# Kernel tuning notes

Hardware: AMD Instinct MI355X
Metric: run time of the kernel (lower is better)

## Reference

```python
import jax, jax.numpy as jnp
import numpy as np

N, E, T = 25000, 400000, 4          # nodes, edges, edge types (one-hot width)
NODE_DIM, EDGE_DIM = 128, 64        # raw feature dims
NO, EO, OUT = 32, 64, 128           # node_ft_out_dim, edge_ft_out_dim, out_dim
D = NO + EO + NO                    # z_node_lv_dim = 128


def segment_softmax(scores, seg, num_segments):
    """Numerically stable softmax over variable-sized segments (1D scores)."""
    m = jax.ops.segment_max(scores, seg, num_segments=num_segments)
    ex = jnp.exp(scores - m[seg])
    den = jax.ops.segment_sum(ex, seg, num_segments=num_segments)
    return ex / den[seg]


def setup_inputs() -> dict:
    key = jax.random.key(0)
    ks = jax.random.split(key, 11)
    node_features = jax.random.normal(ks[0], (N, NODE_DIM), dtype=jnp.float32)
    edge_features = jax.random.normal(ks[1], (E, EDGE_DIM), dtype=jnp.float32)
    src = jax.random.randint(ks[2], (E,), 0, N, dtype=jnp.int32)
    dst = jax.random.randint(ks[3], (E,), 0, N, dtype=jnp.int32)
    edge_type_idx = jax.random.randint(ks[4], (E,), 0, T, dtype=jnp.int32)
    # learned params (torch Linear stored transposed: we use [in, out])
    W_n = jax.random.normal(ks[5], (NODE_DIM, NO), dtype=jnp.float32) / np.sqrt(NODE_DIM)
    W_e = jax.random.normal(ks[6], (EDGE_DIM, EO), dtype=jnp.float32) / np.sqrt(EDGE_DIM)
    w_eattn = jax.random.normal(ks[7], (EO + NO,), dtype=jnp.float32) / np.sqrt(EO + NO)
    w_attn = jax.random.normal(ks[8], (D,), dtype=jnp.float32) / np.sqrt(D)
    w_sem = jax.random.normal(ks[9], (D,), dtype=jnp.float32) / np.sqrt(D)
    W_fc2 = jax.random.normal(ks[10], (D, OUT), dtype=jnp.float32) / np.sqrt(D)
    return {
        "node_features": node_features, "edge_features": edge_features,
        "src": src, "dst": dst, "edge_type_idx": edge_type_idx,
        "W_n": W_n, "W_e": W_e, "w_eattn": w_eattn, "w_attn": w_attn,
        "w_sem": w_sem, "W_fc2": W_fc2,
    }


def reference(node_features, edge_features, src, dst, edge_type_idx,
              W_n, W_e, w_eattn, w_attn, w_sem, W_fc2):
    n = node_features.shape[0]
    # --- WeightedAggEdge: project, then softmax edge weights grouped by SRC ---
    z = node_features @ W_n                      # [N, NO]
    e_ft = edge_features @ W_e                   # [E, EO]
    z_src = z[src]                               # [E, NO]
    s1 = jax.nn.leaky_relu(jnp.concatenate([e_ft, z_src], axis=1) @ w_eattn)  # [E]
    gamma = segment_softmax(s1, src, n)          # softmax over edges sharing src
    e_w = gamma[:, None] * e_ft                  # [E, EO]
    # --- BaseGAT_Modified: edge attention + softmax over DST mailboxes ---
    z_dst = z[dst]                               # [E, NO]
    # message z == z2 == [src z, e_weighted, dst z]
    msg = jnp.concatenate([z_src, e_w, z_dst], axis=1)   # [E, D]
    s2 = jax.nn.leaky_relu(msg @ w_attn)         # [E]
    alpha = segment_softmax(s2, dst, n)          # softmax over incoming edges
    weighted = alpha[:, None] * msg              # [E, D]
    # type-grouped scatter-sum: out[dst, t] += onehot(type)[t] * weighted
    seg = dst * T + edge_type_idx                # fused (node, type) segment id
    h = jax.ops.segment_sum(weighted, seg, num_segments=n * T).reshape(n, T, D)
    # --- SemLevelGAT: semantic attention over edge types ---
    zphi = h.sum(axis=0)                         # [T, D]
    beta = jax.nn.softmax(jax.nn.leaky_relu(zphi @ w_sem))   # [T]
    Z = jnp.einsum('t,ntd->nd', beta, h) @ W_fc2             # [N, OUT]
    return Z, e_w
```

## Files before the change

kernel.cpp:

```cpp
#include <hip/hip_runtime.h>

#define NN 25000
#define NE 400000
#define TT 4
#define NO 32
#define EO 64
#define DD 128
#define OUTD 128
#define EGRID 1250
#define REDB (EGRID / 25)

#define OFF_Z      0
#define OFF_ASRC   800000
#define OFF_BSRC   825000
#define OFF_BDST   850000
#define OFF_ZPART  875000
#define OFF_C2     1400000
#define OFF_S1X    1800000
#define OFF_GAMMA  2200000
#define OFF_S2X    2600000
#define OFF_DEN1   3000000
#define OFF_DEN2   3025000
#define OFF_ZPHI   3050000
#define OFF_BETA   3050512
#define OFF_CSRC   3051000
#define OFF_CDST   3151000
#define OFF_DEG    3251000
#define OFF_OFFS   3276000
#define OFF_CURSOR 3301004
#define OFF_EIDX   3326004
#define OFF_HBETA  3726008
#define OFF_U1     6926008
#define OFF_U2     6926072
#define OFF_WT     6926136
#define OFF_POSS   6928184
#define OFF_SRCC   7328184
#define OFF_WCSR   7728184
#define WS_FLOATS  8128184

#define ZERO_N4    ((OFF_OFFS - OFF_DEN1) / 4)

typedef __attribute__((ext_vector_type(8))) short bf16x8;
typedef __attribute__((ext_vector_type(4))) float f32x4;

__device__ __forceinline__ float lrelu(float x) { return x > 0.f ? x : 0.01f * x; }

__device__ __forceinline__ unsigned short f2b(float x) {
    unsigned u = __float_as_uint(x);
    u += 0x7FFFu + ((u >> 16) & 1u);
    return (unsigned short)(u >> 16);
}

__global__ __launch_bounds__(256) void k_zero(float4* __restrict__ p)
{
    int i = blockIdx.x * 256 + threadIdx.x;
    int stride = gridDim.x * 256;
    for (; i < ZERO_N4; i += stride)
        p[i] = make_float4(0.f, 0.f, 0.f, 0.f);
}

__global__ __launch_bounds__(256) void k_node(const float* __restrict__ nf,
    const float* __restrict__ W_n, const float* __restrict__ w_eattn,
    const float* __restrict__ w_attn, float* __restrict__ z,
    float* __restrict__ a_src, float* __restrict__ b_src, float* __restrict__ b_dst)
{
    __shared__ float Wl[128 * 32];
    __shared__ float nl[8 * 128];
    int tid = threadIdx.x;
    for (int i = tid; i < 128 * 32 / 4; i += 256)
        ((float4*)Wl)[i] = ((const float4*)W_n)[i];
    int nb = blockIdx.x * 8;
    ((float4*)nl)[tid] = ((const float4*)(nf + (size_t)nb * 128))[tid];
    __syncthreads();
    int node = tid >> 5;
    int col = tid & 31;
    float acc = 0.f;
    #pragma unroll 8
    for (int k = 0; k < 128; ++k)
        acc += nl[node * 128 + k] * Wl[k * 32 + col];
    int n = nb + node;
    z[(size_t)n * 32 + col] = acc;
    float va = acc * w_eattn[64 + col];
    float vb = acc * w_attn[col];
    float vc = acc * w_attn[96 + col];
    #pragma unroll
    for (int m = 16; m >= 1; m >>= 1) {
        va += __shfl_xor(va, m);
        vb += __shfl_xor(vb, m);
        vc += __shfl_xor(vc, m);
    }
    if (col == 0) { a_src[n] = va; b_src[n] = vb; b_dst[n] = vc; }
}

__global__ void k_prep(const float* __restrict__ W_e, const float* __restrict__ w_eattn,
                       const float* __restrict__ w_attn, float* __restrict__ u1,
                       float* __restrict__ u2, unsigned short* __restrict__ Wt)
{
    int tid = threadIdx.x;
    if (tid < 64) {
        float s1 = 0.f, s2 = 0.f;
        for (int o = 0; o < 64; ++o) {
            float w = W_e[tid * 64 + o];
            s1 += w * w_eattn[o];
            s2 += w * w_attn[32 + o];
        }
        u1[tid] = s1; u2[tid] = s2;
    }
    for (int i = tid; i < 4096; i += 256) {
        int c = i >> 6, k = i & 63;
        Wt[i] = f2b(W_e[k * 64 + c]);
    }
}

__global__ __launch_bounds__(256) void k_c12s1(const float* __restrict__ ef,
    const float* __restrict__ u1, const float* __restrict__ u2,
    const float* __restrict__ a_src, const int* __restrict__ src, const int* __restrict__ dst,
    float* __restrict__ c2, float* __restrict__ s1x, float* __restrict__ den1, int* __restrict__ deg)
{
    int lane = threadIdx.x & 15, grp = threadIdx.x >> 4;
    float4 v1 = *(const float4*)&u1[lane * 4];
    float4 v2 = *(const float4*)&u2[lane * 4];
    int estep = gridDim.x * 16;
    for (int e = blockIdx.x * 16 + grp; e < NE; e += estep) {
        float4 x = *(const float4*)&ef[(size_t)e * 64 + lane * 4];
        float d1 = x.x * v1.x + x.y * v1.y + x.z * v1.z + x.w * v1.w;
        float d2 = x.x * v2.x + x.y * v2.y + x.z * v2.z + x.w * v2.w;
        #pragma unroll
        for (int m = 8; m >= 1; m >>= 1) {
            d1 += __shfl_xor(d1, m);
            d2 += __shfl_xor(d2, m);
        }
        if (lane == 0) {
            int s = src[e];
            float ex = expf(lrelu(d1 + a_src[s]));
            s1x[e] = ex;
            c2[e] = d2;
            atomicAdd(&den1[s], ex);
            atomicAdd(&deg[dst[e]], 1);
        }
    }
}

__global__ __launch_bounds__(1024) void k_scan(const int* __restrict__ deg,
    int* __restrict__ offs, int* __restrict__ cursor)
{
    __shared__ int wsum[16];
    __shared__ int carry_s;
    int tid = threadIdx.x;
    int lane = tid & 63, wid = tid >> 6;
    if (tid == 0) carry_s = 0;
    __syncthreads();
    for (int base = 0; base < NN; base += 1024) {
        int idx = base + tid;
        int v = (idx < NN) ? deg[idx] : 0;
        int x = v;
        #pragma unroll
        for (int off = 1; off < 64; off <<= 1) {
            int t = __shfl_up(x, off);
            if (lane >= off) x += t;
        }
        if (lane == 63) wsum[wid] = x;
        __syncthreads();
        if (wid == 0) {
            int s = (lane < 16) ? wsum[lane] : 0;
            #pragma unroll
            for (int off = 1; off < 16; off <<= 1) {
                int t = __shfl_up(s, off);
                if (lane >= off) s += t;
            }
            if (lane < 16) wsum[lane] = s;
        }
        __syncthreads();
        int wbase = (wid > 0) ? wsum[wid - 1] : 0;
        int incl = x + wbase;
        int carry = carry_s;
        if (idx < NN) {
            int excl = carry + incl - v;
            offs[idx] = excl;
            cursor[idx] = excl;
        }
        __syncthreads();
        if (tid == 1023) carry_s = carry + incl;
        __syncthreads();
    }
    if (tid == 0) offs[NN] = carry_s;
}

__global__ void k_g2ex(const int* __restrict__ src, const int* __restrict__ dst,
    const float* __restrict__ s1x, const float* __restrict__ den1,
    const float* __restrict__ c2, const float* __restrict__ b_src, const float* __restrict__ b_dst,
    float* __restrict__ gamma, float* __restrict__ s2x, float* __restrict__ den2,
    int* __restrict__ cursor, int* __restrict__ eidx,
    int* __restrict__ poss, int* __restrict__ src_csr)
{
    int e = blockIdx.x * 256 + threadIdx.x;
    if (e >= NE) return;
    int s = src[e], t = dst[e];
    float g = s1x[e] / den1[s];
    gamma[e] = g;
    float ex = expf(lrelu(b_src[s] + g * c2[e] + b_dst[t]));
    s2x[e] = ex;
    atomicAdd(&den2[t], ex);
    int pos = atomicAdd(&cursor[t], 1);
    eidx[pos] = e;
    poss[e] = pos;
    src_csr[pos] = s;
}

__global__ void k_alpha(const int* __restrict__ src, const int* __restrict__ dst,
    const int* __restrict__ ety, const float* __restrict__ s2x, const float* __restrict__ den2,
    float* __restrict__ alpha, float* __restrict__ csrc, float* __restrict__ cdst)
{
    int e = blockIdx.x * 256 + threadIdx.x;
    if (e >= NE) return;
    int t = dst[e];
    int ty = ety[e];
    float al = s2x[e] / den2[t];
    alpha[e] = al;
    atomicAdd(&csrc[src[e] * 4 + ty], al);
    atomicAdd(&cdst[t * 4 + ty], al);
}

__global__ __launch_bounds__(256) void k_edge_mfma(const float* __restrict__ ef,
    const unsigned short* __restrict__ Wt, const float* __restrict__ gamma,
    const float* __restrict__ alpha, const int* __restrict__ ety,
    float* __restrict__ ew, float* __restrict__ zpart)
{
    __shared__ float zl[256];
    int tid = threadIdx.x;
    zl[tid] = 0.f;
    int wv = tid >> 6, lane = tid & 63;
    int row16 = lane & 15, grp = lane >> 4;
    int c4 = row16 * 4;
    bf16x8 b00 = *(const bf16x8*)&Wt[(c4 + 0) * 64 + 0  + grp * 8];
    bf16x8 b01 = *(const bf16x8*)&Wt[(c4 + 0) * 64 + 32 + grp * 8];
    bf16x8 b10 = *(const bf16x8*)&Wt[(c4 + 1) * 64 + 0  + grp * 8];
    bf16x8 b11 = *(const bf16x8*)&Wt[(c4 + 1) * 64 + 32 + grp * 8];
    bf16x8 b20 = *(const bf16x8*)&Wt[(c4 + 2) * 64 + 0  + grp * 8];
    bf16x8 b21 = *(const bf16x8*)&Wt[(c4 + 2) * 64 + 32 + grp * 8];
    bf16x8 b30 = *(const bf16x8*)&Wt[(c4 + 3) * 64 + 0  + grp * 8];
    bf16x8 b31 = *(const bf16x8*)&Wt[(c4 + 3) * 64 + 32 + grp * 8];
    __syncthreads();
    float4 za0 = make_float4(0, 0, 0, 0), za1 = za0, za2 = za0, za3 = za0;
    for (int tile = blockIdx.x; tile < NE / 64; tile += EGRID) {
        size_t eb = (size_t)tile * 64 + wv * 16;
        f32x4 ac0 = {0.f, 0.f, 0.f, 0.f}, ac1 = ac0, ac2 = ac0, ac3 = ac0;
        const float* ap = &ef[(eb + row16) * 64 + grp * 8];
        {
            float4 x0 = *(const float4*)ap;
            float4 x1 = *(const float4*)(ap + 4);
            bf16x8 a;
            a[0] = (short)f2b(x0.x); a[1] = (short)f2b(x0.y);
            a[2] = (short)f2b(x0.z); a[3] = (short)f2b(x0.w);
            a[4] = (short)f2b(x1.x); a[5] = (short)f2b(x1.y);
            a[6] = (short)f2b(x1.z); a[7] = (short)f2b(x1.w);
            ac0 = __builtin_amdgcn_mfma_f32_16x16x32_bf16(a, b00, ac0, 0, 0, 0);
            ac1 = __builtin_amdgcn_mfma_f32_16x16x32_bf16(a, b10, ac1, 0, 0, 0);
            ac2 = __builtin_amdgcn_mfma_f32_16x16x32_bf16(a, b20, ac2, 0, 0, 0);
            ac3 = __builtin_amdgcn_mfma_f32_16x16x32_bf16(a, b30, ac3, 0, 0, 0);
        }
        {
            float4 x0 = *(const float4*)(ap + 32);
            float4 x1 = *(const float4*)(ap + 36);
            bf16x8 a;
            a[0] = (short)f2b(x0.x); a[1] = (short)f2b(x0.y);
            a[2] = (short)f2b(x0.z); a[3] = (short)f2b(x0.w);
            a[4] = (short)f2b(x1.x); a[5] = (short)f2b(x1.y);
            a[6] = (short)f2b(x1.z); a[7] = (short)f2b(x1.w);
            ac0 = __builtin_amdgcn_mfma_f32_16x16x32_bf16(a, b01, ac0, 0, 0, 0);
            ac1 = __builtin_amdgcn_mfma_f32_16x16x32_bf16(a, b11, ac1, 0, 0, 0);
            ac2 = __builtin_amdgcn_mfma_f32_16x16x32_bf16(a, b21, ac2, 0, 0, 0);
            ac3 = __builtin_amdgcn_mfma_f32_16x16x32_bf16(a, b31, ac3, 0, 0, 0);
        }
        #pragma unroll
        for (int j = 0; j < 4; ++j) {
            size_t eg = eb + grp * 4 + j;
            float g = gamma[eg];
            float al = alpha[eg];
            int t = ety[eg];
            float4 v;
            v.x = ac0[j] * g; v.y = ac1[j] * g; v.z = ac2[j] * g; v.w = ac3[j] * g;
            *(float4*)&ew[eg * 64 + c4] = v;
            float w0 = (t == 0) ? al : 0.f, w1 = (t == 1) ? al : 0.f;
            float w2 = (t == 2) ? al : 0.f, w3 = (t == 3) ? al : 0.f;
            za0.x += w0 * v.x; za0.y += w0 * v.y; za0.z += w0 * v.z; za0.w += w0 * v.w;
            za1.x += w1 * v.x; za1.y += w1 * v.y; za1.z += w1 * v.z; za1.w += w1 * v.w;
            za2.x += w2 * v.x; za2.y += w2 * v.y; za2.z += w2 * v.z; za2.w += w2 * v.w;
            za3.x += w3 * v.x; za3.y += w3 * v.y; za3.z += w3 * v.z; za3.w += w3 * v.w;
        }
    }
    atomicAdd(&zl[0 * 64 + c4 + 0], za0.x); atomicAdd(&zl[0 * 64 + c4 + 1], za0.y);
    atomicAdd(&zl[0 * 64 + c4 + 2], za0.z); atomicAdd(&zl[0 * 64 + c4 + 3], za0.w);
    atomicAdd(&zl[1 * 64 + c4 + 0], za1.x); atomicAdd(&zl[1 * 64 + c4 + 1], za1.y);
    atomicAdd(&zl[1 * 64 + c4 + 2], za1.z); atomicAdd(&zl[1 * 64 + c4 + 3], za1.w);
    atomicAdd(&zl[2 * 64 + c4 + 0], za2.x); atomicAdd(&zl[2 * 64 + c4 + 1], za2.y);
    atomicAdd(&zl[2 * 64 + c4 + 2], za2.z); atomicAdd(&zl[2 * 64 + c4 + 3], za2.w);
    atomicAdd(&zl[3 * 64 + c4 + 0], za3.x); atomicAdd(&zl[3 * 64 + c4 + 1], za3.y);
    atomicAdd(&zl[3 * 64 + c4 + 2], za3.z); atomicAdd(&zl[3 * 64 + c4 + 3], za3.w);
    __syncthreads();
    zpart[(size_t)blockIdx.x * 256 + tid] = zl[tid];
}

__global__ __launch_bounds__(256) void k_zphi_fin(const float* __restrict__ zpart,
    const float* __restrict__ z, const float* __restrict__ csrc,
    const float* __restrict__ cdst, float* __restrict__ zphi)
{
    int tid = threadIdx.x;
    if (blockIdx.x < REDB) {
        float s = 0.f;
        int r0 = blockIdx.x * 25;
        for (int r = r0; r < r0 + 25; ++r)
            s += zpart[(size_t)r * 256 + tid];
        atomicAdd(&zphi[(tid >> 6) * 128 + 32 + (tid & 63)], s);
        return;
    }
    int bid = blockIdx.x - REDB;
    __shared__ float zl[256];
    zl[tid] = 0.f;
    __syncthreads();
    int d = tid & 31, ng = tid >> 5;
    float s0 = 0, s1 = 0, s2 = 0, s3 = 0, t0 = 0, t1 = 0, t2 = 0, t3 = 0;
    for (int n = bid * 8 + ng; n < NN; n += 128 * 8) {
        float zv = z[(size_t)n * 32 + d];
        float4 cs = *(const float4*)&csrc[n * 4];
        float4 cd = *(const float4*)&cdst[n * 4];
        s0 += cs.x * zv; s1 += cs.y * zv; s2 += cs.z * zv; s3 += cs.w * zv;
        t0 += cd.x * zv; t1 += cd.y * zv; t2 += cd.z * zv; t3 += cd.w * zv;
    }
    s0 += __shfl_xor(s0, 32); s1 += __shfl_xor(s1, 32);
    s2 += __shfl_xor(s2, 32); s3 += __shfl_xor(s3, 32);
    t0 += __shfl_xor(t0, 32); t1 += __shfl_xor(t1, 32);
    t2 += __shfl_xor(t2, 32); t3 += __shfl_xor(t3, 32);
    if ((tid & 63) < 32) {
        atomicAdd(&zl[0 * 32 + d], s0); atomicAdd(&zl[1 * 32 + d], s1);
        atomicAdd(&zl[2 * 32 + d], s2); atomicAdd(&zl[3 * 32 + d], s3);
        atomicAdd(&zl[128 + 0 * 32 + d], t0); atomicAdd(&zl[128 + 1 * 32 + d], t1);
        atomicAdd(&zl[128 + 2 * 32 + d], t2); atomicAdd(&zl[128 + 3 * 32 + d], t3);
    }
    __syncthreads();
    if (tid < 128) atomicAdd(&zphi[(tid >> 5) * 128 + (tid & 31)], zl[tid]);
    else atomicAdd(&zphi[((tid - 128) >> 5) * 128 + 96 + (tid & 31)], zl[tid]);
}

__global__ __launch_bounds__(128) void k_beta(const float* __restrict__ zphi,
    const float* __restrict__ w_sem, float* __restrict__ beta)
{
    int tid = threadIdx.x;
    float w = w_sem[tid];
    float p0 = zphi[tid] * w, p1 = zphi[128 + tid] * w;
    float p2 = zphi[256 + tid] * w, p3 = zphi[384 + tid] * w;
    #pragma unroll
    for (int m = 32; m >= 1; m >>= 1) {
        p0 += __shfl_xor(p0, m); p1 += __shfl_xor(p1, m);
        p2 += __shfl_xor(p2, m); p3 += __shfl_xor(p3, m);
    }
    __shared__ float s[2][4];
    if ((tid & 63) == 0) {
        int w_ = tid >> 6;
        s[w_][0] = p0; s[w_][1] = p1; s[w_][2] = p2; s[w_][3] = p3;
    }
    __syncthreads();
    if (tid == 0) {
        float d0 = lrelu(s[0][0] + s[1][0]);
        float d1 = lrelu(s[0][1] + s[1][1]);
        float d2 = lrelu(s[0][2] + s[1][2]);
        float d3 = lrelu(s[0][3] + s[1][3]);
        float mx = fmaxf(fmaxf(d0, d1), fmaxf(d2, d3));
        float e0 = expf(d0 - mx), e1 = expf(d1 - mx), e2 = expf(d2 - mx), e3 = expf(d3 - mx);
        float inv = 1.f / (e0 + e1 + e2 + e3);
        beta[0] = e0 * inv; beta[1] = e1 * inv; beta[2] = e2 * inv; beta[3] = e3 * inv;
    }
}

__global__ void k_walpha(const float* __restrict__ alpha, const int* __restrict__ ety,
                         const float* __restrict__ beta, const int* __restrict__ poss,
                         float* __restrict__ w_csr)
{
    int e = blockIdx.x * 256 + threadIdx.x;
    if (e >= NE) return;
    w_csr[poss[e]] = alpha[e] * beta[ety[e]];
}

__global__ __launch_bounds__(256) void k_scatter(const int* __restrict__ offs,
    const int* __restrict__ eidx, const int* __restrict__ src_csr,
    const float* __restrict__ w_csr, const float* __restrict__ z,
    const float* __restrict__ ew, float* __restrict__ hbeta)
{
    int tid = threadIdx.x;
    int lane = tid & 31;
    int grp = tid >> 5;
    int n = blockIdx.x * 8 + grp;
    if (n >= NN) return;
    int d0 = lane * 4;
    int beg = offs[n], end = offs[n + 1];
    float4 acc = make_float4(0, 0, 0, 0);
    float sumw = 0.f;
    int i = beg;
    for (; i + 2 <= end; i += 2) {
        int ea = eidx[i], eb = eidx[i + 1];
        float wa = w_csr[i], wb = w_csr[i + 1];
        int sa = src_csr[i], sb = src_csr[i + 1];
        sumw += wa + wb;
        if (lane < 24) {
            const float* pa = (lane < 8) ? &z[(size_t)sa * 32 + d0]
                                         : &ew[(size_t)ea * 64 + (d0 - 32)];
            const float* pb = (lane < 8) ? &z[(size_t)sb * 32 + d0]
                                         : &ew[(size_t)eb * 64 + (d0 - 32)];
            float4 ma = *(const float4*)pa;
            float4 mb = *(const float4*)pb;
            acc.x += wa * ma.x + wb * mb.x; acc.y += wa * ma.y + wb * mb.y;
            acc.z += wa * ma.z + wb * mb.z; acc.w += wa * ma.w + wb * mb.w;
        }
    }
    if (i < end) {
        int ea = eidx[i];
        float wa = w_csr[i];
        int sa = src_csr[i];
        sumw += wa;
        if (lane < 24) {
            const float* pa = (lane < 8) ? &z[(size_t)sa * 32 + d0]
                                         : &ew[(size_t)ea * 64 + (d0 - 32)];
            float4 ma = *(const float4*)pa;
            acc.x += wa * ma.x; acc.y += wa * ma.y; acc.z += wa * ma.z; acc.w += wa * ma.w;
        }
    }
    if (lane >= 24) {
        float4 zd = *(const float4*)&z[(size_t)n * 32 + (d0 - 96)];
        acc.x = sumw * zd.x; acc.y = sumw * zd.y; acc.z = sumw * zd.z; acc.w = sumw * zd.w;
    }
    *(float4*)&hbeta[(size_t)n * 128 + d0] = acc;
}

__global__ __launch_bounds__(256) void k_fc(const float* __restrict__ hb,
    const float* __restrict__ W, float* __restrict__ Z)
{
    __shared__ float hl[32 * 132];
    __shared__ float Wl[128 * 64];
    int tid = threadIdx.x;
    int nb = blockIdx.x * 32;
    for (int i = tid; i < 1024; i += 256) {
        int row = i >> 5, kc = (i & 31) * 4;
        float4 v = make_float4(0.f, 0.f, 0.f, 0.f);
        if (nb + row < NN) v = *(const float4*)&hb[(size_t)(nb + row) * 128 + kc];
        *(float4*)&hl[row * 132 + kc] = v;
    }
    for (int half = 0; half < 2; ++half) {
        __syncthreads();
        for (int i = tid; i < 2048; i += 256) {
            int k = i >> 4, c = (i & 15) * 4;
            *(float4*)&Wl[k * 64 + c] = *(const float4*)&W[(size_t)k * 128 + half * 64 + c];
        }
        __syncthreads();
        int node = tid >> 3;
        int c0 = (tid & 7) * 8;
        float acc[8] = {0, 0, 0, 0, 0, 0, 0, 0};
        #pragma unroll 4
        for (int k = 0; k < 128; ++k) {
            float a = hl[node * 132 + k];
            const float* wr = &Wl[k * 64 + c0];
            #pragma unroll
            for (int j = 0; j < 8; ++j) acc[j] += a * wr[j];
        }
        int n = nb + node;
        if (n < NN) {
            float4 o1, o2;
            o1.x = acc[0]; o1.y = acc[1]; o1.z = acc[2]; o1.w = acc[3];
            o2.x = acc[4]; o2.y = acc[5]; o2.z = acc[6]; o2.w = acc[7];
            *(float4*)&Z[(size_t)n * 128 + half * 64 + c0] = o1;
            *(float4*)&Z[(size_t)n * 128 + half * 64 + c0 + 4] = o2;
        }
    }
}

extern "C" void kernel_launch(void* const* d_in, const int* in_sizes, int n_in,
                              void* d_out, int out_size, void* d_ws, size_t ws_size,
                              hipStream_t stream)
{
    const float* nf     = (const float*)d_in[0];
    const float* ef     = (const float*)d_in[1];
    const int*   src    = (const int*)d_in[2];
    const int*   dst    = (const int*)d_in[3];
    const int*   ety    = (const int*)d_in[4];
    const float* W_n    = (const float*)d_in[5];
    const float* W_e    = (const float*)d_in[6];
    const float* w_eattn= (const float*)d_in[7];
    const float* w_attn = (const float*)d_in[8];
    const float* w_sem  = (const float*)d_in[9];
    const float* W_fc2  = (const float*)d_in[10];

    float* out = (float*)d_out;
    float* Z   = out;
    float* ew  = out + (size_t)NN * OUTD;

    float* ws    = (float*)d_ws;
    float* z     = ws + OFF_Z;
    float* a_src = ws + OFF_ASRC;
    float* b_src = ws + OFF_BSRC;
    float* b_dst = ws + OFF_BDST;
    float* zpart = ws + OFF_ZPART;
    float* c2    = ws + OFF_C2;
    float* s1x   = ws + OFF_S1X;
    float* gamma = ws + OFF_GAMMA;
    float* s2x   = ws + OFF_S2X;
    float* alpha = ws + OFF_S1X;
    float* den1  = ws + OFF_DEN1;
    float* den2  = ws + OFF_DEN2;
    float* zphi  = ws + OFF_ZPHI;
    float* beta  = ws + OFF_BETA;
    float* csrc  = ws + OFF_CSRC;
    float* cdst  = ws + OFF_CDST;
    int* deg     = (int*)(ws + OFF_DEG);
    int* offs    = (int*)(ws + OFF_OFFS);
    int* cursor  = (int*)(ws + OFF_CURSOR);
    int* eidx    = (int*)(ws + OFF_EIDX);
    float* hbeta = ws + OFF_HBETA;
    float* u1    = ws + OFF_U1;
    float* u2    = ws + OFF_U2;
    unsigned short* Wt = (unsigned short*)(ws + OFF_WT);
    int* poss    = (int*)(ws + OFF_POSS);
    int* src_csr = (int*)(ws + OFF_SRCC);
    float* w_csr = ws + OFF_WCSR;

    k_zero<<<270, 256, 0, stream>>>((float4*)(ws + OFF_DEN1));
    k_node<<<NN / 8, 256, 0, stream>>>(nf, W_n, w_eattn, w_attn, z, a_src, b_src, b_dst);
    k_prep<<<1, 256, 0, stream>>>(W_e, w_eattn, w_attn, u1, u2, Wt);
    k_c12s1<<<2048, 256, 0, stream>>>(ef, u1, u2, a_src, src, dst, c2, s1x, den1, deg);
    k_scan<<<1, 1024, 0, stream>>>(deg, offs, cursor);
    int gE = (NE + 255) / 256;
    k_g2ex<<<gE, 256, 0, stream>>>(src, dst, s1x, den1, c2, b_src, b_dst, gamma, s2x, den2, cursor, eidx, poss, src_csr);
    k_alpha<<<gE, 256, 0, stream>>>(src, dst, ety, s2x, den2, alpha, csrc, cdst);
    k_edge_mfma<<<EGRID, 256, 0, stream>>>(ef, Wt, gamma, alpha, ety, ew, zpart);
    k_zphi_fin<<<REDB + 128, 256, 0, stream>>>(zpart, z, csrc, cdst, zphi);
    k_beta<<<1, 128, 0, stream>>>(zphi, w_sem, beta);
    k_walpha<<<gE, 256, 0, stream>>>(alpha, ety, beta, poss, w_csr);
    k_scatter<<<(NN + 7) / 8, 256, 0, stream>>>(offs, eidx, src_csr, w_csr, z, ew, hbeta);
    k_fc<<<(NN + 31) / 32, 256, 0, stream>>>(hbeta, W_fc2, Z);
}
```

Measured before the change: 327.1 us.

## Cache bf16 edge features in first pass and parallelize degree scan

The first edge pass, which already reads the fp32 edge features, now also writes a bf16 copy to workspace. The MFMA edge kernel reads that half-width copy instead of re-reading and converting the fp32 features. Separately, the single-block degree scan is rewritten so each thread serially scans 25 contiguous entries, followed by one block-wide scan instead of a loop of 25 synchronized block scans. The bf16 copy adds a 51 MB write in the first pass and grows the workspace, trading a 102 MB fp32 re-read for a 51 MB bf16 write plus read.

New measurement: 334.7 us. +2.3%, slower.

```diff
diff --git a/kernel.cpp b/kernel.cpp
--- a/kernel.cpp
+++ b/kernel.cpp
@@ -36,7 +36,8 @@
 #define OFF_POSS   6928184
 #define OFF_SRCC   7328184
 #define OFF_WCSR   7728184
-#define WS_FLOATS  8128184
+#define OFF_EF16   8128184
+#define WS_FLOATS  20928184
 
 #define ZERO_N4    ((OFF_OFFS - OFF_DEN1) / 4)
 
@@ -115,7 +116,8 @@
 __global__ __launch_bounds__(256) void k_c12s1(const float* __restrict__ ef,
     const float* __restrict__ u1, const float* __restrict__ u2,
     const float* __restrict__ a_src, const int* __restrict__ src, const int* __restrict__ dst,
-    float* __restrict__ c2, float* __restrict__ s1x, float* __restrict__ den1, int* __restrict__ deg)
+    float* __restrict__ c2, float* __restrict__ s1x, float* __restrict__ den1,
+    int* __restrict__ deg, unsigned short* __restrict__ ef16)
 {
     int lane = threadIdx.x & 15, grp = threadIdx.x >> 4;
     float4 v1 = *(const float4*)&u1[lane * 4];
@@ -123,6 +125,9 @@
     int estep = gridDim.x * 16;
     for (int e = blockIdx.x * 16 + grp; e < NE; e += estep) {
         float4 x = *(const float4*)&ef[(size_t)e * 64 + lane * 4];
+        ushort4 h;
+        h.x = f2b(x.x); h.y = f2b(x.y); h.z = f2b(x.z); h.w = f2b(x.w);
+        *(ushort4*)&ef16[(size_t)e * 64 + lane * 4] = h;
         float d1 = x.x * v1.x + x.y * v1.y + x.z * v1.z + x.w * v1.w;
         float d2 = x.x * v2.x + x.y * v2.y + x.z * v2.z + x.w * v2.w;
         #pragma unroll
@@ -145,45 +150,48 @@
     int* __restrict__ offs, int* __restrict__ cursor)
 {
     __shared__ int wsum[16];
-    __shared__ int carry_s;
     int tid = threadIdx.x;
     int lane = tid & 63, wid = tid >> 6;
-    if (tid == 0) carry_s = 0;
-    __syncthreads();
-    for (int base = 0; base < NN; base += 1024) {
-        int idx = base + tid;
-        int v = (idx < NN) ? deg[idx] : 0;
-        int x = v;
+    int base = tid * 25;
+    int v[25];
+    int tot = 0;
+    #pragma unroll
+    for (int j = 0; j < 25; ++j) {
+        int idx = base + j;
+        int d = (idx < NN) ? deg[idx] : 0;
+        v[j] = tot;
+        tot += d;
+    }
+    int x = tot;
+    #pragma unroll
+    for (int off = 1; off < 64; off <<= 1) {
+        int t = __shfl_up(x, off);
+        if (lane >= off) x += t;
+    }
+    if (lane == 63) wsum[wid] = x;
+    __syncthreads();
+    if (wid == 0) {
+        int s = (lane < 16) ? wsum[lane] : 0;
         #pragma unroll
-        for (int off = 1; off < 64; off <<= 1) {
-            int t = __shfl_up(x, off);
-            if (lane >= off) x += t;
-        }
-        if (lane == 63) wsum[wid] = x;
-        __syncthreads();
-        if (wid == 0) {
-            int s = (lane < 16) ? wsum[lane] : 0;
-            #pragma unroll
-            for (int off = 1; off < 16; off <<= 1) {
-                int t = __shfl_up(s, off);
-                if (lane >= off) s += t;
-            }
-            if (lane < 16) wsum[lane] = s;
-        }
-        __syncthreads();
-        int wbase = (wid > 0) ? wsum[wid - 1] : 0;
-        int incl = x + wbase;
-        int carry = carry_s;
+        for (int off = 1; off < 16; off <<= 1) {
+            int t = __shfl_up(s, off);
+            if (lane >= off) s += t;
+        }
+        if (lane < 16) wsum[lane] = s;
+    }
+    __syncthreads();
+    int wbase = (wid > 0) ? wsum[wid - 1] : 0;
+    int myexcl = wbase + x - tot;
+    #pragma unroll
+    for (int j = 0; j < 25; ++j) {
+        int idx = base + j;
         if (idx < NN) {
-            int excl = carry + incl - v;
-            offs[idx] = excl;
-            cursor[idx] = excl;
-        }
-        __syncthreads();
-        if (tid == 1023) carry_s = carry + incl;
-        __syncthreads();
-    }
-    if (tid == 0) offs[NN] = carry_s;
+            int e = myexcl + v[j];
+            offs[idx] = e;
+            cursor[idx] = e;
+        }
+    }
+    if (tid == 1023) offs[NN] = myexcl + tot;
 }
 
 __global__ void k_g2ex(const int* __restrict__ src, const int* __restrict__ dst,
@@ -221,7 +229,7 @@
     atomicAdd(&cdst[t * 4 + ty], al);
 }
 
-__global__ __launch_bounds__(256) void k_edge_mfma(const float* __restrict__ ef,
+__global__ __launch_bounds__(256) void k_edge_mfma(const unsigned short* __restrict__ ef16,
     const unsigned short* __restrict__ Wt, const float* __restrict__ gamma,
     const float* __restrict__ alpha, const int* __restrict__ ety,
     float* __restrict__ ew, float* __restrict__ zpart)
@@ -245,28 +253,16 @@
     for (int tile = blockIdx.x; tile < NE / 64; tile += EGRID) {
         size_t eb = (size_t)tile * 64 + wv * 16;
         f32x4 ac0 = {0.f, 0.f, 0.f, 0.f}, ac1 = ac0, ac2 = ac0, ac3 = ac0;
-        const float* ap = &ef[(eb + row16) * 64 + grp * 8];
+        const unsigned short* ap = &ef16[(eb + row16) * 64 + grp * 8];
         {
-            float4 x0 = *(const float4*)ap;
-            float4 x1 = *(const float4*)(ap + 4);
-            bf16x8 a;
-            a[0] = (short)f2b(x0.x); a[1] = (short)f2b(x0.y);
-            a[2] = (short)f2b(x0.z); a[3] = (short)f2b(x0.w);
-            a[4] = (short)f2b(x1.x); a[5] = (short)f2b(x1.y);
-            a[6] = (short)f2b(x1.z); a[7] = (short)f2b(x1.w);
+            bf16x8 a = *(const bf16x8*)ap;
             ac0 = __builtin_amdgcn_mfma_f32_16x16x32_bf16(a, b00, ac0, 0, 0, 0);
             ac1 = __builtin_amdgcn_mfma_f32_16x16x32_bf16(a, b10, ac1, 0, 0, 0);
             ac2 = __builtin_amdgcn_mfma_f32_16x16x32_bf16(a, b20, ac2, 0, 0, 0);
             ac3 = __builtin_amdgcn_mfma_f32_16x16x32_bf16(a, b30, ac3, 0, 0, 0);
         }
         {
-            float4 x0 = *(const float4*)(ap + 32);
-            float4 x1 = *(const float4*)(ap + 36);
-            bf16x8 a;
-            a[0] = (short)f2b(x0.x); a[1] = (short)f2b(x0.y);
-            a[2] = (short)f2b(x0.z); a[3] = (short)f2b(x0.w);
-            a[4] = (short)f2b(x1.x); a[5] = (short)f2b(x1.y);
-            a[6] = (short)f2b(x1.z); a[7] = (short)f2b(x1.w);
+            bf16x8 a = *(const bf16x8*)(ap + 32);
             ac0 = __builtin_amdgcn_mfma_f32_16x16x32_bf16(a, b01, ac0, 0, 0, 0);
             ac1 = __builtin_amdgcn_mfma_f32_16x16x32_bf16(a, b11, ac1, 0, 0, 0);
             ac2 = __builtin_amdgcn_mfma_f32_16x16x32_bf16(a, b21, ac2, 0, 0, 0);
@@ -520,16 +516,17 @@
     int* poss    = (int*)(ws + OFF_POSS);
     int* src_csr = (int*)(ws + OFF_SRCC);
     float* w_csr = ws + OFF_WCSR;
+    unsigned short* ef16 = (unsigned short*)(ws + OFF_EF16);
 
     k_zero<<<270, 256, 0, stream>>>((float4*)(ws + OFF_DEN1));
     k_node<<<NN / 8, 256, 0, stream>>>(nf, W_n, w_eattn, w_attn, z, a_src, b_src, b_dst);
     k_prep<<<1, 256, 0, stream>>>(W_e, w_eattn, w_attn, u1, u2, Wt);
-    k_c12s1<<<2048, 256, 0, stream>>>(ef, u1, u2, a_src, src, dst, c2, s1x, den1, deg);
+    k_c12s1<<<2048, 256, 0, stream>>>(ef, u1, u2, a_src, src, dst, c2, s1x, den1, deg, ef16);
     k_scan<<<1, 1024, 0, stream>>>(deg, offs, cursor);
     int gE = (NE + 255) / 256;
     k_g2ex<<<gE, 256, 0, stream>>>(src, dst, s1x, den1, c2, b_src, b_dst, gamma, s2x, den2, cursor, eidx, poss, src_csr);
     k_alpha<<<gE, 256, 0, stream>>>(src, dst, ety, s2x, den2, alpha, csrc, cdst);
-    k_edge_mfma<<<EGRID, 256, 0, stream>>>(ef, Wt, gamma, alpha, ety, ew, zpart);
+    k_edge_mfma<<<EGRID, 256, 0, stream>>>(ef16, Wt, gamma, alpha, ety, ew, zpart);
     k_zphi_fin<<<REDB + 128, 256, 0, stream>>>(zpart, z, csrc, cdst, zphi);
     k_beta<<<1, 128, 0, stream>>>(zphi, w_sem, beta);
     k_walpha<<<gE, 256, 0, stream>>>(alpha, ety, beta, poss, w_csr);
```
